# Performance work log

Hardware: AMD Instinct MI355X
Metric: run time of the kernel (lower is better)

## Reference

```python
import jax, jax.numpy as jnp
import numpy as np

D = 1024

def setup_inputs() -> dict:
    key = jax.random.key(0)
    ks = jax.random.split(key, 7)
    s = 1.0 / np.sqrt(D)
    x = jax.random.normal(ks[0], (4, 4096, D), dtype=jnp.float32)
    Wi = jax.random.uniform(ks[1], (2 * D, D), jnp.float32, -s, s)   # in_proj weight [2D, D]
    bi = jax.random.uniform(ks[2], (2 * D,), jnp.float32, -s, s)
    Wc = jax.random.uniform(ks[3], (D, 1, 3), jnp.float32, -0.577, 0.577)  # depthwise conv [D,1,3]
    bc = jax.random.uniform(ks[4], (D,), jnp.float32, -0.577, 0.577)
    Wo = jax.random.uniform(ks[5], (D, D), jnp.float32, -s, s)       # out_proj weight [D, D]
    bo = jax.random.uniform(ks[6], (D,), jnp.float32, -s, s)
    return {"x": x, "Wi": Wi, "bi": bi, "Wc": Wc, "bc": bc, "Wo": Wo, "bo": bo}

def _depthwise_conv1d(v, Wc, bc):
    # v: [B, L, D] -> NCH [B, D, L]; kernel [D, 1, 3] (OIH), groups = D; pad 1 both sides
    y = jax.lax.conv_general_dilated(
        v.transpose(0, 2, 1), Wc,
        window_strides=(1,), padding=[(1, 1)],
        dimension_numbers=("NCH", "OIH", "NCH"),
        feature_group_count=v.shape[-1])
    return y.transpose(0, 2, 1) + bc  # [B, L, D]

def reference(x, Wi, bi, Wc, bc, Wo, bo):
    uv = jnp.einsum("bld,ed->ble", x, Wi) + bi        # [B, L, 2D]
    u, v = jnp.split(uv, 2, axis=-1)                   # each [B, L, D]
    y = _depthwise_conv1d(v, Wc, bc)
    y = jax.nn.silu(y) * u                             # fused gate
    return jnp.einsum("bld,ed->ble", y, Wo) + bo       # [B, L, D]
```

## Files before the change

kernel.cpp:

```cpp
#include <hip/hip_runtime.h>
#include <math.h>


typedef __attribute__((ext_vector_type(8))) short short8;
typedef __attribute__((ext_vector_type(4))) float floatx4;

__device__ __forceinline__ float b2f(short s) {
    unsigned int u = ((unsigned int)(unsigned short)s) << 16;
    float f;
    __builtin_memcpy(&f, &u, 4);
    return f;
}

__device__ __forceinline__ short f2b(float f) {
    unsigned int u;
    __builtin_memcpy(&u, &f, 4);
    u += 0x7fffu + ((u >> 16) & 1u);
    return (short)(u >> 16);
}

__device__ __forceinline__ void gl_lds16(const short* g, short* l) {
    __builtin_amdgcn_global_load_lds(
        (const __attribute__((address_space(1))) unsigned int*)g,
        (__attribute__((address_space(3))) unsigned int*)l,
        16, 0, 0);
}

__global__ __launch_bounds__(256) void cvt_all(
    const float* __restrict__ x, const float* __restrict__ Wi,
    const float* __restrict__ Wo, short* __restrict__ xb,
    short* __restrict__ Wib, short* __restrict__ Wob)
{
    constexpr int n1 = 16384 * 1024 / 8;
    constexpr int n2 = 2048 * 1024 / 8;
    constexpr int n3 = 1024 * 1024 / 8;
    int i = blockIdx.x * 256 + threadIdx.x;
    const float* src;
    short* dst;
    int j;
    if (i < n1)           { src = x;  dst = xb;  j = i; }
    else if (i < n1 + n2) { src = Wi; dst = Wib; j = i - n1; }
    else if (i < n1 + n2 + n3) { src = Wo; dst = Wob; j = i - n1 - n2; }
    else return;
    float4 a = ((const float4*)src)[2 * j];
    float4 b = ((const float4*)src)[2 * j + 1];
    short8 o;
    o[0] = f2b(a.x); o[1] = f2b(a.y); o[2] = f2b(a.z); o[3] = f2b(a.w);
    o[4] = f2b(b.x); o[5] = f2b(b.y); o[6] = f2b(b.z); o[7] = f2b(b.w);
    ((short8*)dst)[j] = o;
}

#define GB_TILE(SLOT, NSLOT, P, NP, WAIT, ST, PREF)                           \
  {                                                                           \
    asm volatile(WAIT ::: "memory");                                          \
    __builtin_amdgcn_s_barrier();                                             \
    asm volatile("" ::: "memory");                                            \
    if ((ST) >= 0) {                                                          \
        gl_lds16(gA + (size_t)(ST) * 32, lA0 + ((ST) & 3) * 8192);            \
        gl_lds16(gA + (size_t)(ST) * 32 + (size_t)16 * lda,                   \
                 lA0 + ((ST) & 3) * 8192 + 512);                              \
    }                                                                         \
    short8 a1_[4];                                                            \
    _Pragma("unroll") for (int mi = 0; mi < 4; mi++)                          \
        a1_[mi] = *(const short8*)&As[(SLOT) * 8192 + aBase + (4 + mi) * 512];\
    __builtin_amdgcn_s_setprio(1);                                            \
    _Pragma("unroll") for (int mi = 0; mi < 4; mi++)                          \
      _Pragma("unroll") for (int ni = 0; ni < 4; ni++)                        \
        acc[mi][ni] = __builtin_amdgcn_mfma_f32_16x16x32_bf16(                \
            a0[P][mi], bvv[P][ni], acc[mi][ni], 0, 0, 0);                     \
    __builtin_amdgcn_s_setprio(0);                                            \
    if ((ST) >= 0) {                                                          \
        gl_lds16(gB + (size_t)(ST) * 32, lB0 + ((ST) & 3) * 8192);            \
        gl_lds16(gB + (size_t)(ST) * 32 + (size_t)16 * ldb,                   \
                 lB0 + ((ST) & 3) * 8192 + 512);                              \
    }                                                                         \
    if (PREF) {                                                               \
      _Pragma("unroll") for (int ni = 0; ni < 4; ni++)                        \
        bvv[NP][ni] = *(const short8*)&Bs[(NSLOT) * 8192 + bBase + ni * 512]; \
      _Pragma("unroll") for (int mi = 0; mi < 4; mi++)                        \
        a0[NP][mi] = *(const short8*)&As[(NSLOT) * 8192 + aBase + mi * 512];  \
    }                                                                         \
    __builtin_amdgcn_s_setprio(1);                                            \
    _Pragma("unroll") for (int mi = 0; mi < 4; mi++)                          \
      _Pragma("unroll") for (int ni = 0; ni < 4; ni++)                        \
        acc[4 + mi][ni] = __builtin_amdgcn_mfma_f32_16x16x32_bf16(            \
            a1_[mi], bvv[P][ni], acc[4 + mi][ni], 0, 0, 0);                   \
    __builtin_amdgcn_s_setprio(0);                                            \
  }

template <bool OUTF32>
__global__ __launch_bounds__(512, 2) void gemm_bt(
    const short* __restrict__ A, const short* __restrict__ B,
    const float* __restrict__ bias, void* __restrict__ Cv,
    int lda, int ldb, int ldc)
{
    __shared__ __attribute__((aligned(16))) short As[4 * 8192];
    __shared__ __attribute__((aligned(16))) short Bs[4 * 8192];

    const int tid  = threadIdx.x;
    const int wave = tid >> 6;
    const int lane = tid & 63;

    const int nwg = gridDim.x * gridDim.y;
    const int f   = blockIdx.y * gridDim.x + blockIdx.x;
    const int nf  = (f & 7) * (nwg >> 3) + (f >> 3);
    const int mBase = (nf / gridDim.x) * 256;
    const int nBase = (nf % gridDim.x) * 256;

    floatx4 acc[8][4];
#pragma unroll
    for (int i = 0; i < 8; i++)
#pragma unroll
        for (int j = 0; j < 4; j++) acc[i][j] = {0.f, 0.f, 0.f, 0.f};

    const int srow = lane >> 2;
    const int sg   = ((lane & 3) ^ ((srow >> 1) & 3)) * 8;
    const short* gA = A + (size_t)(mBase + wave * 32 + srow) * lda + sg;
    const short* gB = B + (size_t)(nBase + wave * 32 + srow) * ldb + sg;
    short* lA0 = &As[wave * 1024];
    short* lB0 = &Bs[wave * 1024];

    const int fRow = lane & 15;
    const int lg   = lane >> 4;
    const int pg8  = (lg ^ ((fRow >> 1) & 3)) * 8;
    const int mq   = (wave >> 2) * 128;
    const int nq   = (wave & 3) * 64;
    const int aBase = (mq + fRow) * 32 + pg8;
    const int bBase = (nq + fRow) * 32 + pg8;

    short8 bvv[2][4], a0[2][4];

#pragma unroll
    for (int p = 0; p < 3; p++) {
        gl_lds16(gA + (size_t)p * 32, lA0 + p * 8192);
        gl_lds16(gA + (size_t)p * 32 + (size_t)16 * lda, lA0 + p * 8192 + 512);
        gl_lds16(gB + (size_t)p * 32, lB0 + p * 8192);
        gl_lds16(gB + (size_t)p * 32 + (size_t)16 * ldb, lB0 + p * 8192 + 512);
    }
    asm volatile("s_waitcnt vmcnt(8)" ::: "memory");
    __builtin_amdgcn_s_barrier();
    asm volatile("" ::: "memory");
#pragma unroll
    for (int ni = 0; ni < 4; ni++)
        bvv[0][ni] = *(const short8*)&Bs[bBase + ni * 512];
#pragma unroll
    for (int mi = 0; mi < 4; mi++)
        a0[0][mi] = *(const short8*)&As[aBase + mi * 512];

    for (int tb = 0; tb < 28; tb += 4) {
        GB_TILE(0, 1, 0, 1, "s_waitcnt vmcnt(4)", tb + 3, 1)
        GB_TILE(1, 2, 1, 0, "s_waitcnt vmcnt(4)", tb + 4, 1)
        GB_TILE(2, 3, 0, 1, "s_waitcnt vmcnt(4)", tb + 5, 1)
        GB_TILE(3, 0, 1, 0, "s_waitcnt vmcnt(4)", tb + 6, 1)
    }
    GB_TILE(0, 1, 0, 1, "s_waitcnt vmcnt(4)", 31, 1)
    GB_TILE(1, 2, 1, 0, "s_waitcnt vmcnt(4)", -1, 1)
    GB_TILE(2, 3, 0, 1, "s_waitcnt vmcnt(0)", -1, 1)
    GB_TILE(3, 0, 1, 0, "s_waitcnt vmcnt(0)", -1, 0)

    const int colq = lane & 15;
    const int rowq = lg * 4;
#pragma unroll
    for (int ni = 0; ni < 4; ni++) {
        const int col = nBase + nq + ni * 16 + colq;
        const float bsv = bias[col];
#pragma unroll
        for (int mi = 0; mi < 8; mi++) {
            const int row = mBase + mq + mi * 16 + rowq;
#pragma unroll
            for (int r = 0; r < 4; r++) {
                float v = acc[mi][ni][r] + bsv;
                if (OUTF32)
                    ((float*)Cv)[(size_t)(row + r) * ldc + col] = v;
                else
                    ((short*)Cv)[(size_t)(row + r) * ldc + col] = f2b(v);
            }
        }
    }
}

__global__ __launch_bounds__(256) void conv_gate(
    const short* __restrict__ uv, const float* __restrict__ Wc,
    const float* __restrict__ bc, short* __restrict__ yb)
{
    const int idx = blockIdx.x * 256 + threadIdx.x;
    const int d8 = idx & 127;
    const int m  = idx >> 7;
    const int l  = m & 4095;
    const int d  = d8 * 8;

    float w[24];
#pragma unroll
    for (int q = 0; q < 6; q++)
        *(float4*)&w[q * 4] = ((const float4*)(Wc + d * 3))[q];
    float bcv[8];
    *(float4*)&bcv[0] = ((const float4*)(bc + d))[0];
    *(float4*)&bcv[4] = ((const float4*)(bc + d))[1];

    const size_t rowu = (size_t)m * 2048 + d;
    const size_t rowv = rowu + 1024;

    const short8 z = {0, 0, 0, 0, 0, 0, 0, 0};
    const short8 us = *(const short8*)(uv + rowu);
    const short8 vc = *(const short8*)(uv + rowv);
    const short8 vm = (l > 0)    ? *(const short8*)(uv + rowv - 2048) : z;
    const short8 vp = (l < 4095) ? *(const short8*)(uv + rowv + 2048) : z;

    short8 outv;
#pragma unroll
    for (int j = 0; j < 8; j++) {
        float y = b2f(vm[j]) * w[j * 3 + 0]
                + b2f(vc[j]) * w[j * 3 + 1]
                + b2f(vp[j]) * w[j * 3 + 2]
                + bcv[j];
        float sil = y / (1.0f + expf(-y));
        outv[j] = f2b(sil * b2f(us[j]));
    }
    *(short8*)(yb + (size_t)m * 1024 + d) = outv;
}

extern "C" void kernel_launch(void* const* d_in, const int* in_sizes, int n_in,
                              void* d_out, int out_size, void* d_ws, size_t ws_size,
                              hipStream_t stream)
{
    const float* x  = (const float*)d_in[0];
    const float* Wi = (const float*)d_in[1];
    const float* bi = (const float*)d_in[2];
    const float* Wc = (const float*)d_in[3];
    const float* bc = (const float*)d_in[4];
    const float* Wo = (const float*)d_in[5];
    const float* bo = (const float*)d_in[6];
    float* out = (float*)d_out;

    short* wsS = (short*)d_ws;
    short* uv  = wsS;
    short* xb  = uv + (size_t)16384 * 2048;
    short* Wib = xb + (size_t)16384 * 1024;
    short* Wob = Wib + (size_t)2048 * 1024;

    dim3 blk(256);
    dim3 blkG(512);

    constexpr int nCvt = (16384 * 1024 + 2048 * 1024 + 1024 * 1024) / 8;
    cvt_all<<<(nCvt + 255) / 256, blk, 0, stream>>>(x, Wi, Wo, xb, Wib, Wob);

    dim3 g1(2048 / 256, 16384 / 256);
    gemm_bt<false><<<g1, blkG, 0, stream>>>(xb, Wib, bi, uv, 1024, 1024, 2048);

    conv_gate<<<(16384 * 128) / 256, blk, 0, stream>>>(uv, Wc, bc, xb);

    dim3 g2(1024 / 256, 16384 / 256);
    gemm_bt<true><<<g2, blkG, 0, stream>>>(xb, Wob, bo, out, 1024, 1024, 1024);
}
```

Measured before the change: 299.5 us.

## Restructure GEMM main loop into ping-pong barrier schedule with per-tile LDS loads

Replaces the register double-buffered fragment prefetch in the bf16 GEMM main loop with a schedule that loads fragments for the current tile at its start. Each half-tile MFMA cluster is now fenced by sched_barrier and s_barrier, in a ping-pong style so the waves of a workgroup alternate memory and compute phases. Global-to-LDS wait counts are loosened, allowing more loads to stay in flight. This removes register pressure from the double-buffered fragments. The cost is extra barriers per tile and exposed LDS read latency before the MFMAs.

Result: faster. 291.3 us (-2.7%).

```diff
diff --git a/kernel.cpp b/kernel.cpp
--- a/kernel.cpp
+++ b/kernel.cpp
@@ -50,42 +50,49 @@
     ((short8*)dst)[j] = o;
 }
 
-#define GB_TILE(SLOT, NSLOT, P, NP, WAIT, ST, PREF)                           \
+#define GB_TILE(SLOT, S3, WAIT, ST)                                           \
   {                                                                           \
-    asm volatile(WAIT ::: "memory");                                          \
-    __builtin_amdgcn_s_barrier();                                             \
-    asm volatile("" ::: "memory");                                            \
+    short8 bvv[4], a0[4];                                                     \
+    _Pragma("unroll") for (int ni = 0; ni < 4; ni++)                          \
+        bvv[ni] = *(const short8*)&Bs[(SLOT) * 8192 + bBase + ni * 512];      \
+    _Pragma("unroll") for (int mi = 0; mi < 4; mi++)                          \
+        a0[mi] = *(const short8*)&As[(SLOT) * 8192 + aBase + mi * 512];       \
     if ((ST) >= 0) {                                                          \
-        gl_lds16(gA + (size_t)(ST) * 32, lA0 + ((ST) & 3) * 8192);            \
+        gl_lds16(gA + (size_t)(ST) * 32, lA0 + (S3) * 8192);                  \
         gl_lds16(gA + (size_t)(ST) * 32 + (size_t)16 * lda,                   \
-                 lA0 + ((ST) & 3) * 8192 + 512);                              \
+                 lA0 + (S3) * 8192 + 512);                                    \
     }                                                                         \
-    short8 a1_[4];                                                            \
-    _Pragma("unroll") for (int mi = 0; mi < 4; mi++)                          \
-        a1_[mi] = *(const short8*)&As[(SLOT) * 8192 + aBase + (4 + mi) * 512];\
+    __builtin_amdgcn_sched_barrier(0);                                        \
+    __builtin_amdgcn_s_barrier();                                             \
+    asm volatile("s_waitcnt lgkmcnt(0)" ::: "memory");                        \
+    __builtin_amdgcn_sched_barrier(0);                                        \
     __builtin_amdgcn_s_setprio(1);                                            \
     _Pragma("unroll") for (int mi = 0; mi < 4; mi++)                          \
       _Pragma("unroll") for (int ni = 0; ni < 4; ni++)                        \
         acc[mi][ni] = __builtin_amdgcn_mfma_f32_16x16x32_bf16(                \
-            a0[P][mi], bvv[P][ni], acc[mi][ni], 0, 0, 0);                     \
+            a0[mi], bvv[ni], acc[mi][ni], 0, 0, 0);                           \
     __builtin_amdgcn_s_setprio(0);                                            \
+    __builtin_amdgcn_s_barrier();                                             \
+    short8 a1[4];                                                             \
+    _Pragma("unroll") for (int mi = 0; mi < 4; mi++)                          \
+        a1[mi] = *(const short8*)&As[(SLOT) * 8192 + aBase + (4 + mi) * 512]; \
     if ((ST) >= 0) {                                                          \
-        gl_lds16(gB + (size_t)(ST) * 32, lB0 + ((ST) & 3) * 8192);            \
+        gl_lds16(gB + (size_t)(ST) * 32, lB0 + (S3) * 8192);                  \
         gl_lds16(gB + (size_t)(ST) * 32 + (size_t)16 * ldb,                   \
-                 lB0 + ((ST) & 3) * 8192 + 512);                              \
+                 lB0 + (S3) * 8192 + 512);                                    \
     }                                                                         \
-    if (PREF) {                                                               \
-      _Pragma("unroll") for (int ni = 0; ni < 4; ni++)                        \
-        bvv[NP][ni] = *(const short8*)&Bs[(NSLOT) * 8192 + bBase + ni * 512]; \
-      _Pragma("unroll") for (int mi = 0; mi < 4; mi++)                        \
-        a0[NP][mi] = *(const short8*)&As[(NSLOT) * 8192 + aBase + mi * 512];  \
-    }                                                                         \
+    asm volatile(WAIT ::: "memory");                                          \
+    __builtin_amdgcn_sched_barrier(0);                                        \
+    __builtin_amdgcn_s_barrier();                                             \
+    asm volatile("s_waitcnt lgkmcnt(0)" ::: "memory");                        \
+    __builtin_amdgcn_sched_barrier(0);                                        \
     __builtin_amdgcn_s_setprio(1);                                            \
     _Pragma("unroll") for (int mi = 0; mi < 4; mi++)                          \
       _Pragma("unroll") for (int ni = 0; ni < 4; ni++)                        \
         acc[4 + mi][ni] = __builtin_amdgcn_mfma_f32_16x16x32_bf16(            \
-            a1_[mi], bvv[P][ni], acc[4 + mi][ni], 0, 0, 0);                   \
+            a1[mi], bvv[ni], acc[4 + mi][ni], 0, 0, 0);                       \
     __builtin_amdgcn_s_setprio(0);                                            \
+    __builtin_amdgcn_s_barrier();                                             \
   }
 
 template <bool OUTF32>
@@ -128,8 +135,6 @@
     const int aBase = (mq + fRow) * 32 + pg8;
     const int bBase = (nq + fRow) * 32 + pg8;
 
-    short8 bvv[2][4], a0[2][4];
-
 #pragma unroll
     for (int p = 0; p < 3; p++) {
         gl_lds16(gA + (size_t)p * 32, lA0 + p * 8192);
@@ -140,23 +145,17 @@
     asm volatile("s_waitcnt vmcnt(8)" ::: "memory");
     __builtin_amdgcn_s_barrier();
     asm volatile("" ::: "memory");
-#pragma unroll
-    for (int ni = 0; ni < 4; ni++)
-        bvv[0][ni] = *(const short8*)&Bs[bBase + ni * 512];
-#pragma unroll
-    for (int mi = 0; mi < 4; mi++)
-        a0[0][mi] = *(const short8*)&As[aBase + mi * 512];
 
     for (int tb = 0; tb < 28; tb += 4) {
-        GB_TILE(0, 1, 0, 1, "s_waitcnt vmcnt(4)", tb + 3, 1)
-        GB_TILE(1, 2, 1, 0, "s_waitcnt vmcnt(4)", tb + 4, 1)
-        GB_TILE(2, 3, 0, 1, "s_waitcnt vmcnt(4)", tb + 5, 1)
-        GB_TILE(3, 0, 1, 0, "s_waitcnt vmcnt(4)", tb + 6, 1)
-    }
-    GB_TILE(0, 1, 0, 1, "s_waitcnt vmcnt(4)", 31, 1)
-    GB_TILE(1, 2, 1, 0, "s_waitcnt vmcnt(4)", -1, 1)
-    GB_TILE(2, 3, 0, 1, "s_waitcnt vmcnt(0)", -1, 1)
-    GB_TILE(3, 0, 1, 0, "s_waitcnt vmcnt(0)", -1, 0)
+        GB_TILE(0, 3, "s_waitcnt vmcnt(8)", tb + 3)
+        GB_TILE(1, 0, "s_waitcnt vmcnt(8)", tb + 4)
+        GB_TILE(2, 1, "s_waitcnt vmcnt(8)", tb + 5)
+        GB_TILE(3, 2, "s_waitcnt vmcnt(8)", tb + 6)
+    }
+    GB_TILE(0, 3, "s_waitcnt vmcnt(8)", 31)
+    GB_TILE(1, 0, "s_waitcnt vmcnt(4)", -1)
+    GB_TILE(2, 1, "s_waitcnt vmcnt(0)", -1)
+    GB_TILE(3, 2, "s_waitcnt vmcnt(0)", -1)
 
     const int colq = lane & 15;
     const int rowq = lg * 4;
```
